# Performance work log

Measured on AMD Instinct MI355X. Metric: run time of the kernel, lower is better.

## Reference

```python
import jax, jax.numpy as jnp
import numpy as np

B, N, C = 4, 48 * 64, 256
H, W = 48, 64


def _positional_encodings(batch, dtype=jnp.float32):
    # (x^2, y^2, xy, x, y, 1) encoding; matches get_positional_encodings with intrinsics=None
    ys = jnp.linspace(-1.0, 1.0, H, dtype=dtype)
    xs = jnp.linspace(-1.0, 1.0, W, dtype=dtype)
    p3 = jnp.tile(ys, W)            # [N] : ys repeated W times (torch .repeat(B, w))
    p4 = jnp.repeat(xs, H)          # [N] : each x repeated H times (repeat_interleave)
    pos = jnp.stack([p3 * p3, p4 * p4, p3 * p4, p3, p4, jnp.ones_like(p3)], axis=-1)  # [N,6]
    return jnp.broadcast_to(pos, (batch, N, 6))


def setup_inputs() -> dict:
    key = jax.random.key(0)
    k1, k2, k3, k4 = jax.random.split(key, 4)
    x1 = jax.random.normal(k1, (B, N, C), dtype=jnp.float32)
    x2 = jax.random.normal(k2, (B, N, C), dtype=jnp.float32)
    corr = jax.random.normal(k3, (B, 1, H, W, H, W), dtype=jnp.float32)
    W_proj = jax.random.normal(k4, (C + 6, C), dtype=jnp.float32) * (1.0 / np.sqrt(C + 6))
    b_proj = jnp.zeros((C,), dtype=jnp.float32)
    return {"x1": x1, "x2": x2, "corr": corr, "W_proj": W_proj, "b_proj": b_proj}


def reference(x1, x2, corr, W_proj, b_proj):
    b, n, c = x1.shape
    a = corr.reshape(b, n, n)                      # squeeze(1) + double flatten
    # dual softmax (row-wise * column-wise)
    s_row = jax.nn.softmax(a, axis=-1)
    s_col = jax.nn.softmax(a, axis=-2)
    attn_f1 = s_row * s_col                        # [B,N,N]
    attn_f2 = jnp.swapaxes(attn_f1, -2, -1)        # softmax(a^T,-1)*softmax(a^T,-2) == attn_f1^T

    pos = _positional_encodings(b, dtype=x1.dtype)
    v1 = jnp.concatenate([x1, pos], axis=2)        # [B,N,C+6]
    v2 = jnp.concatenate([x2, pos], axis=2)

    # bilinear products v^T @ attn @ v  -> [B, C+6, C+6]
    fund1 = jnp.einsum('bnc,bnm,bmd->bcd', v1, attn_f1, v1)
    fund2 = jnp.einsum('bnc,bnm,bmd->bcd', v2, attn_f2, v2)

    fund1 = jnp.swapaxes(fund1, -2, -1)
    fund2 = jnp.swapaxes(fund2, -2, -1)

    out1 = fund1 @ W_proj + b_proj                 # proj_fundamental
    out2 = fund2 @ W_proj + b_proj
    return (out2, out1)                            # (fundamental_2, fundamental_1)
```

## Files before the change

kernel.cpp:

```cpp
#include <hip/hip_runtime.h>
#include <math.h>

#define NB 4
#define NN 3072
#define NC 256
#define CP 262
#define KG 384
#define XW 528
#define MD 272
#define K3S 8
#define HH 48
#define WW 64
#define LOG2E 1.4426950408889634f

typedef short short8 __attribute__((ext_vector_type(8)));
typedef short short4v __attribute__((ext_vector_type(4)));
typedef float f32x4 __attribute__((ext_vector_type(4)));
typedef unsigned int uint4v __attribute__((ext_vector_type(4)));

__device__ __forceinline__ float fexp2(float x) {
#if __has_builtin(__builtin_amdgcn_exp2f)
    return __builtin_amdgcn_exp2f(x);
#else
    return __exp2f(x);
#endif
}

__device__ __forceinline__ void bsplit(float v, short& h, short& l) {
    unsigned u = __float_as_uint(v);
    h = (short)(u >> 16);
    float r = v - __uint_as_float(u & 0xFFFF0000u);
    l = (short)(__float_as_uint(r) >> 16);
}

__device__ __forceinline__ void fma4(float4& c, float a, float4 b) {
    c.x = fmaf(a, b.x, c.x);
    c.y = fmaf(a, b.y, c.y);
    c.z = fmaf(a, b.z, c.z);
    c.w = fmaf(a, b.w, c.w);
}

__global__ __launch_bounds__(256) void k_stats(const float* __restrict__ corr,
                                               const float* __restrict__ x1,
                                               const float* __restrict__ x2,
                                               float* __restrict__ pM, float* __restrict__ pS,
                                               float* __restrict__ rmS, float* __restrict__ irs,
                                               short* __restrict__ Xh, short* __restrict__ Xl) {
    int bid = blockIdx.x;
    int t = threadIdx.x;
    if (bid < 384) {
        int cx = bid % 12;
        int b = (bid / 12) & 3;
        int ch = bid / 48;
        int m = cx * 256 + t;
        const float* p = corr + (size_t)b * NN * NN + (size_t)ch * 384 * NN + m;
        float mx[4], s[4];
#pragma unroll
        for (int i = 0; i < 4; i++) { mx[i] = -3.4e38f; s[i] = 0.f; }
        for (int r = 0; r < 384; r += 4) {
#pragma unroll
            for (int i = 0; i < 4; i++) {
                float x = p[(size_t)(r + i) * NN];
                float mn = fmaxf(mx[i], x);
                s[i] = s[i] * __expf(mx[i] - mn) + __expf(x - mn);
                mx[i] = mn;
            }
        }
        float mn01 = fmaxf(mx[0], mx[1]);
        float s01 = s[0] * __expf(mx[0] - mn01) + s[1] * __expf(mx[1] - mn01);
        float mn23 = fmaxf(mx[2], mx[3]);
        float s23 = s[2] * __expf(mx[2] - mn23) + s[3] * __expf(mx[3] - mn23);
        float mnA = fmaxf(mn01, mn23);
        float sA = s01 * __expf(mn01 - mnA) + s23 * __expf(mn23 - mnA);
        pM[((size_t)ch * NB + b) * NN + m] = mnA;
        pS[((size_t)ch * NB + b) * NN + m] = sA;
    } else if (bid < 3456) {
        int rid = bid - 384;
        int b = rid / 768;
        int r0 = (rid - b * 768) * 4;
        int w = t >> 6, l = t & 63;
        int n = r0 + w;
        const float4* p = (const float4*)(corr + ((size_t)b * NN + n) * NN);
        float4 v[12];
        float m = -3.4e38f;
#pragma unroll
        for (int i = 0; i < 12; i++) {
            v[i] = p[l + i * 64];
            m = fmaxf(m, fmaxf(fmaxf(v[i].x, v[i].y), fmaxf(v[i].z, v[i].w)));
        }
#pragma unroll
        for (int off = 1; off < 64; off <<= 1) m = fmaxf(m, __shfl_xor(m, off));
        float s = 0.f;
#pragma unroll
        for (int i = 0; i < 12; i++)
            s += __expf(v[i].x - m) + __expf(v[i].y - m) + __expf(v[i].z - m) + __expf(v[i].w - m);
#pragma unroll
        for (int off = 1; off < 64; off <<= 1) s += __shfl_xor(s, off);
        if (l == 0) {
            rmS[b * NN + n] = m * LOG2E;
            irs[b * NN + n] = 1.f / s;
        }
    } else {
        int id = (bid - 3456) * 256 + t;
        int col = id % XW;
        int rest = id / XW;
        int kg = rest % KG;
        int b = rest / KG;
        short* ph = Xh + (size_t)id * 8;
        short* pl = Xl + (size_t)id * 8;
        if (col < 512) {
            const float* src = (col < 256 ? x1 : x2) + ((size_t)b * NN + kg * 8) * NC + (col & 255);
#pragma unroll
            for (int j = 0; j < 8; j++) {
                short hs, ls;
                bsplit(src[(size_t)j * NC], hs, ls);
                ph[j] = hs; pl[j] = ls;
            }
        } else {
            int c = col - 512;
#pragma unroll
            for (int j = 0; j < 8; j++) {
                int k = kg * 8 + j;
                int ip4 = k / HH;
                int ip3 = k - ip4 * HH;
                float p3 = -1.f + 2.f * (float)ip3 / 47.f;
                float p4 = -1.f + 2.f * (float)ip4 / 63.f;
                float v = 0.f;
                if (c == 0) v = p3 * p3;
                else if (c == 1) v = p4 * p4;
                else if (c == 2) v = p3 * p4;
                else if (c == 3) v = p3;
                else if (c == 4) v = p4;
                else if (c == 5) v = 1.f;
                short hs, ls;
                bsplit(v, hs, ls);
                ph[j] = hs; pl[j] = ls;
            }
        }
    }
}

struct SMemMain {
    unsigned AH[2][96 * 32];
    unsigned AL[2][96 * 32];
    float ccsh[NN];
};
union SMemU {
    SMemMain m;
    float pdump[8 * 64 * 24];
};

#define LOAD_B2(PH, PL, BHF, BLF)                                           \
    {                                                                        \
        BHF[0] = *(const short8*)(PH);                                       \
        BHF[1] = *(const short8*)((PH) + 128);                               \
        BLF[0] = *(const short8*)(PL);                                       \
        BLF[1] = *(const short8*)((PL) + 128);                               \
    }

#define READ_AFRAGS6(BUFH, BUFL, UNIT, AHF, ALF)                             \
    {                                                                        \
        _Pragma("unroll") for (int fr_ = 0; fr_ < 6; fr_++) {                \
            int rowr_ = fr_ * 16 + row16;                                    \
            int uidx_ = rowr_ * 32 + (((UNIT) ^ (rowr_ & 7)) << 2);          \
            AHF[fr_] = *(const short8*)&(BUFH)[uidx_];                       \
            ALF[fr_] = *(const short8*)&(BUFL)[uidx_];                       \
        }                                                                    \
    }

#define MFMA_CLUSTER62(AHF, ALF, BHF, BLF)                                                         \
    {                                                                                              \
        _Pragma("unroll") for (int fr_ = 0; fr_ < 6; fr_++)                                        \
        _Pragma("unroll") for (int i_ = 0; i_ < 2; i_++)                                           \
            acc[fr_][i_] = __builtin_amdgcn_mfma_f32_16x16x32_bf16(AHF[fr_], BHF[i_], acc[fr_][i_], 0, 0, 0); \
        _Pragma("unroll") for (int fr_ = 0; fr_ < 6; fr_++)                                        \
        _Pragma("unroll") for (int i_ = 0; i_ < 2; i_++)                                           \
            acc[fr_][i_] = __builtin_amdgcn_mfma_f32_16x16x32_bf16(AHF[fr_], BLF[i_], acc[fr_][i_], 0, 0, 0); \
        _Pragma("unroll") for (int fr_ = 0; fr_ < 6; fr_++)                                        \
        _Pragma("unroll") for (int i_ = 0; i_ < 2; i_++)                                           \
            acc[fr_][i_] = __builtin_amdgcn_mfma_f32_16x16x32_bf16(ALF[fr_], BHF[i_], acc[fr_][i_], 0, 0, 0); \
    }

#define POS_CLUSTER6(AHF, ALF, PBH, PBL)                                                           \
    {                                                                                              \
        _Pragma("unroll") for (int fr_ = 0; fr_ < 6; fr_++) {                                      \
            accP[fr_] = __builtin_amdgcn_mfma_f32_16x16x32_bf16(AHF[fr_], (PBH), accP[fr_], 0, 0, 0); \
            accP[fr_] = __builtin_amdgcn_mfma_f32_16x16x32_bf16(AHF[fr_], (PBL), accP[fr_], 0, 0, 0); \
            accP[fr_] = __builtin_amdgcn_mfma_f32_16x16x32_bf16(ALF[fr_], (PBH), accP[fr_], 0, 0, 0); \
        }                                                                                          \
    }

#define STAGE_A(DSTH, DSTL, PC)                                                                   \
    {                                                                                             \
        f32x4 ccv0 = *(const f32x4*)&ccsh[(PC) * 64 + g * 16];                                    \
        f32x4 ccv1 = *(const f32x4*)&ccsh[(PC) * 64 + g * 16 + 4];                                \
        f32x4 ccv2 = *(const f32x4*)&ccsh[(PC) * 64 + g * 16 + 8];                                \
        f32x4 ccv3 = *(const f32x4*)&ccsh[(PC) * 64 + g * 16 + 12];                               \
        float ev[16];                                                                             \
        _Pragma("unroll") for (int q_ = 0; q_ < 4; q_++) {                                        \
            ev[q_]      = fexp2(fmaf(C2, cr[0][q_], rmn) - ccv0[q_]);                             \
            ev[4 + q_]  = fexp2(fmaf(C2, cr[1][q_], rmn) - ccv1[q_]);                             \
            ev[8 + q_]  = fexp2(fmaf(C2, cr[2][q_], rmn) - ccv2[q_]);                             \
            ev[12 + q_] = fexp2(fmaf(C2, cr[3][q_], rmn) - ccv3[q_]);                             \
        }                                                                                         \
        uint4v hi0, hi1, lo0, lo1;                                                                \
        _Pragma("unroll") for (int q_ = 0; q_ < 4; q_++) {                                        \
            unsigned u0 = __float_as_uint(ev[2 * q_]);                                            \
            unsigned u1 = __float_as_uint(ev[2 * q_ + 1]);                                        \
            hi0[q_] = __builtin_amdgcn_perm(u1, u0, 0x07060302u);                                 \
            float r0_ = ev[2 * q_] - __uint_as_float(u0 & 0xffff0000u);                           \
            float r1_ = ev[2 * q_ + 1] - __uint_as_float(u1 & 0xffff0000u);                       \
            lo0[q_] = __builtin_amdgcn_perm(__float_as_uint(r1_), __float_as_uint(r0_), 0x07060302u); \
            unsigned v0 = __float_as_uint(ev[8 + 2 * q_]);                                        \
            unsigned v1 = __float_as_uint(ev[8 + 2 * q_ + 1]);                                    \
            hi1[q_] = __builtin_amdgcn_perm(v1, v0, 0x07060302u);                                 \
            float t0_ = ev[8 + 2 * q_] - __uint_as_float(v0 & 0xffff0000u);                       \
            float t1_ = ev[8 + 2 * q_ + 1] - __uint_as_float(v1 & 0xffff0000u);                   \
            lo1[q_] = __builtin_amdgcn_perm(__float_as_uint(t1_), __float_as_uint(t0_), 0x07060302u); \
        }                                                                                         \
        *(uint4v*)&(DSTH)[widx0] = hi0;                                                           \
        *(uint4v*)&(DSTH)[widx1] = hi1;                                                           \
        *(uint4v*)&(DSTL)[widx0] = lo0;                                                           \
        *(uint4v*)&(DSTL)[widx1] = lo1;                                                           \
    }

__global__ __launch_bounds__(512, 2) void k2_mfma(const float* __restrict__ corr,
        const short* __restrict__ Xh, const short* __restrict__ Xl,
        const float* __restrict__ rmS, const float* __restrict__ irs,
        const float* __restrict__ pM, const float* __restrict__ pS,
        short* __restrict__ Zh, short* __restrict__ Zl) {
    __shared__ SMemU sm;
    float* ccsh = sm.m.ccsh;

    const float C2 = 2.f * LOG2E;
    const size_t BSTEP = (size_t)4 * XW * 8;

    int bid = blockIdx.x;
    int xcd = bid & 7, sub = bid >> 3;
    int b = xcd >> 1;
    int which = sub & 1;
    int rowblk = (xcd & 1) + ((sub >> 1) << 1);
    int n0 = rowblk * 96;

    int t = threadIdx.x;
    int w = t >> 6, l = t & 63;
    int row16 = l & 15, slot = l >> 4;
    bool doPos = (which == 0);
    bool writer = (t < 384);
    int wrow = t >> 2, g = t & 3;
    int widx0 = wrow * 32 + (((2 * g) ^ (wrow & 7)) << 2);
    int widx1 = wrow * 32 + (((2 * g + 1) ^ (wrow & 7)) << 2);

    for (int c = t; c < NN; c += 512) {
        float mx = -3.4e38f, s = 0.f;
#pragma unroll
        for (int ch = 0; ch < 8; ch++) {
            float m2 = pM[(size_t)ch * NB * NN + b * NN + c];
            float s2 = pS[(size_t)ch * NB * NN + b * NN + c];
            float mn = fmaxf(mx, m2);
            s = s * __expf(mx - mn) + s2 * __expf(m2 - mn);
            mx = mn;
        }
        ccsh[c] = fmaf(mx, LOG2E, __log2f(s));
    }

    const float* corrR = corr;
    float rmn = 0.f;
    if (writer) {
        corrR = corr + ((size_t)b * NN + n0 + wrow) * NN + g * 16;
        rmn = -rmS[b * NN + n0 + wrow];
    }

    int col0 = which * 256 + w * 32 + row16;
    const short* bh = Xh + ((size_t)(b * KG + slot) * XW + col0) * 8;
    const short* bl = Xl + ((size_t)(b * KG + slot) * XW + col0) * 8;

    f32x4 acc[6][2];
    f32x4 accP[6];
    const f32x4 zz = {0.f, 0.f, 0.f, 0.f};
#pragma unroll
    for (int fr = 0; fr < 6; fr++) {
        acc[fr][0] = zz; acc[fr][1] = zz; accP[fr] = zz;
    }

    short8 BhA[2], BlA[2], BhB[2], BlB[2];
    short8 P0h = {0,0,0,0,0,0,0,0}, P0l = P0h, P1h = P0h, P1l = P0h;
    LOAD_B2(bh, bl, BhA, BlA);

    f32x4 cr[4];
    __syncthreads();
    if (writer) {
#pragma unroll
        for (int q = 0; q < 4; q++) cr[q] = *(const f32x4*)(corrR + q * 4);
        STAGE_A(sm.m.AH[0], sm.m.AL[0], 0);
#pragma unroll
        for (int q = 0; q < 4; q++) cr[q] = *(const f32x4*)(corrR + 64 + q * 4);
    }
    asm volatile("s_waitcnt lgkmcnt(0)" ::: "memory");
    __builtin_amdgcn_s_barrier();

    int cur = 0;
    for (int p = 0; p < 48; ++p) {
        const unsigned* AHc = &sm.m.AH[cur][0];
        const unsigned* ALc = &sm.m.AL[cur][0];
        unsigned* AHn = &sm.m.AH[cur ^ 1][0];
        unsigned* ALn = &sm.m.AL[cur ^ 1][0];
        bool duty = doPos && (w == (p & 7));
        if (duty) {
            size_t o0 = ((size_t)(b * KG + p * 8 + slot) * XW + 512 + row16) * 8;
            P0h = *(const short8*)(Xh + o0);
            P0l = *(const short8*)(Xl + o0);
            P1h = *(const short8*)(Xh + o0 + BSTEP);
            P1l = *(const short8*)(Xl + o0 + BSTEP);
        }
        short8 Ah[6], Al[6];
        READ_AFRAGS6(AHc, ALc, slot, Ah, Al);
        bh += BSTEP; bl += BSTEP;
        LOAD_B2(bh, bl, BhB, BlB);
        MFMA_CLUSTER62(Ah, Al, BhA, BlA);
        if (duty) POS_CLUSTER6(Ah, Al, P0h, P0l);
        READ_AFRAGS6(AHc, ALc, 4 + slot, Ah, Al);
        if (p < 47) {
            bh += BSTEP; bl += BSTEP;
            LOAD_B2(bh, bl, BhA, BlA);
        }
        if (writer) {
            int pc = (p + 1 < 48) ? p + 1 : 47;
            STAGE_A(AHn, ALn, pc);
            int pn = (p + 2 < 48) ? p + 2 : 47;
#pragma unroll
            for (int q = 0; q < 4; q++) cr[q] = *(const f32x4*)(corrR + pn * 64 + q * 4);
        }
        MFMA_CLUSTER62(Ah, Al, BhB, BlB);
        if (duty) POS_CLUSTER6(Ah, Al, P1h, P1l);
        asm volatile("s_waitcnt lgkmcnt(0)" ::: "memory");
        __builtin_amdgcn_s_barrier();
        cur ^= 1;
    }

#pragma unroll
    for (int fr = 0; fr < 6; fr++) {
        f32x4 sv = *(const f32x4*)(irs + b * NN + n0 + fr * 16 + slot * 4);
        int kgz = rowblk * 12 + fr * 2 + (slot >> 1);
        int jb = (slot & 1) << 2;
#pragma unroll
        for (int i = 0; i < 2; i++) {
            int colv = which * 256 + w * 32 + i * 16 + row16;
            size_t off = ((size_t)(b * KG + kgz) * XW + colv) * 8 + jb;
            short4v zh, zl;
#pragma unroll
            for (int r = 0; r < 4; r++) {
                float vv = acc[fr][i][r] * sv[r];
                short hs, ls; bsplit(vv, hs, ls);
                zh[r] = hs; zl[r] = ls;
            }
            *(short4v*)(Zh + off) = zh;
            *(short4v*)(Zl + off) = zl;
        }
    }
    if (doPos) {
#pragma unroll
        for (int fr = 0; fr < 6; fr++)
            *(f32x4*)&sm.pdump[(size_t)(w * 64 + l) * 24 + fr * 4] = accP[fr];
    }
    __syncthreads();
    if (doPos && t < 384) {
        int fr = t >> 6, ll = t & 63;
        int sl = ll >> 4, r16 = ll & 15;
        f32x4 s = zz;
#pragma unroll
        for (int ww = 0; ww < 8; ww++)
            s += *(const f32x4*)&sm.pdump[(size_t)(ww * 64 + ll) * 24 + fr * 4];
        f32x4 sv = *(const f32x4*)(irs + b * NN + n0 + fr * 16 + sl * 4);
        int kgz = rowblk * 12 + fr * 2 + (sl >> 1);
        int jb = (sl & 1) << 2;
        size_t off = ((size_t)(b * KG + kgz) * XW + 512 + r16) * 8 + jb;
        short4v zh, zl;
#pragma unroll
        for (int r = 0; r < 4; r++) {
            float vv = s[r] * sv[r];
            short hs, ls; bsplit(vv, hs, ls);
            zh[r] = hs; zl[r] = ls;
        }
        *(short4v*)(Zh + off) = zh;
        *(short4v*)(Zl + off) = zl;
    }
}

__global__ __launch_bounds__(256) void k3_mfma(const short* __restrict__ Xh, const short* __restrict__ Xl,
                                               const short* __restrict__ Zh, const short* __restrict__ Zl,
                                               float* __restrict__ Mpart) {
    int tile = blockIdx.x;
    int rt = tile / 3, ct = tile % 3;
    int mb = blockIdx.y;
    int mat = mb >> 2, b = mb & 3;
    int split = blockIdx.z;

    const int O0[4] = {0, 6, 12, 17};
    int r0f = O0[rt], rNf = O0[rt + 1] - r0f;
    int c0f = O0[ct], cNf = O0[ct + 1] - c0f;

    int t = threadIdx.x;
    int w = t >> 6, l = t & 63;
    int row16 = l & 15, slot = l >> 4;
    int wr = w >> 1, wc = w & 1;
    int rh = (rNf + 1) >> 1;
    int rbeg = r0f + (wr ? rh : 0);
    int rcnt = wr ? (rNf - rh) : rh;
    int chh = (cNf + 1) >> 1;
    int cbeg = c0f + (wc ? chh : 0);
    int ccnt = wc ? (cNf - chh) : chh;

    const short *Ah_, *Al_, *Bh_, *Bl_;
    int abase, bbase;
    if (mat == 0) { Ah_ = Xh; Al_ = Xl; Bh_ = Zh; Bl_ = Zl; abase = 0; bbase = 0; }
    else          { Ah_ = Zh; Al_ = Zl; Bh_ = Xh; Bl_ = Xl; abase = 256; bbase = 256; }

    int acol[3], bcol[3];
#pragma unroll
    for (int i = 0; i < 3; i++) {
        int fa = rbeg + i;
        acol[i] = ((fa < 16) ? (abase + fa * 16) : 512) + row16;
        int fb = cbeg + i;
        bcol[i] = ((fb < 16) ? (bbase + fb * 16) : 512) + row16;
    }

    f32x4 acc[3][3];
    const f32x4 zz = {0.f, 0.f, 0.f, 0.f};
#pragma unroll
    for (int i = 0; i < 3; i++)
#pragma unroll
        for (int j = 0; j < 3; j++) acc[i][j] = zz;

    for (int it = 0; it < 12; it++) {
        int kg = split * 48 + it * 4 + slot;
        size_t base = (size_t)(b * KG + kg) * XW;
        short8 Ah[3], Al[3], Bhf[3], Blf[3];
#pragma unroll
        for (int i = 0; i < 3; i++) {
            if (i < rcnt) {
                Ah[i] = *(const short8*)(Ah_ + (base + acol[i]) * 8);
                Al[i] = *(const short8*)(Al_ + (base + acol[i]) * 8);
            }
            if (i < ccnt) {
                Bhf[i] = *(const short8*)(Bh_ + (base + bcol[i]) * 8);
                Blf[i] = *(const short8*)(Bl_ + (base + bcol[i]) * 8);
            }
        }
#pragma unroll
        for (int i = 0; i < 3; i++) {
            if (i < rcnt) {
#pragma unroll
                for (int j = 0; j < 3; j++) {
                    if (j < ccnt) {
                        acc[i][j] = __builtin_amdgcn_mfma_f32_16x16x32_bf16(Ah[i], Bhf[j], acc[i][j], 0, 0, 0);
                        acc[i][j] = __builtin_amdgcn_mfma_f32_16x16x32_bf16(Al[i], Bhf[j], acc[i][j], 0, 0, 0);
                        acc[i][j] = __builtin_amdgcn_mfma_f32_16x16x32_bf16(Ah[i], Blf[j], acc[i][j], 0, 0, 0);
                    }
                }
            }
        }
    }

    float* Mp = Mpart + (size_t)(mb * K3S + split) * (MD * MD);
#pragma unroll
    for (int i = 0; i < 3; i++) {
        if (i < rcnt) {
#pragma unroll
            for (int j = 0; j < 3; j++) {
                if (j < ccnt) {
                    int r = (rbeg + i) * 16 + slot * 4;
                    int c = (cbeg + j) * 16 + row16;
#pragma unroll
                    for (int q = 0; q < 4; q++)
                        Mp[(size_t)(r + q) * MD + c] = acc[i][j][q];
                }
            }
        }
    }
}

__global__ __launch_bounds__(256) void k_mcombine(const float* __restrict__ Mpart, float* __restrict__ M) {
    const int per = MD * MD;
    int f4 = blockIdx.x * 256 + threadIdx.x;
    if (f4 >= (8 * per) / 4) return;
    int e = f4 * 4;
    int mb = e / per;
    int off = e - mb * per;
    const float* src = Mpart + (size_t)mb * K3S * per + off;
    float4 s = make_float4(0.f, 0.f, 0.f, 0.f);
#pragma unroll
    for (int sp = 0; sp < K3S; sp++) {
        float4 v = *(const float4*)(src + (size_t)sp * per);
        s.x += v.x; s.y += v.y; s.z += v.z; s.w += v.w;
    }
    *(float4*)(M + (size_t)mb * per + off) = s;
}

__global__ __launch_bounds__(256) void k4_proj(const float* __restrict__ M, const float* __restrict__ Wp,
                                               const float* __restrict__ bp, float* __restrict__ out) {
    int i0 = blockIdx.x * 16;
    int b = blockIdx.y;
    int mat = blockIdx.z;
    const float* Mp = M + (size_t)(mat * 4 + b) * (MD * MD);
    int t = threadIdx.x;
    int jt = t & 63, it = t >> 6;
    int j = jt * 4;
    float4 a0 = make_float4(0.f, 0.f, 0.f, 0.f), a1 = a0, a2 = a0, a3 = a0;
#pragma unroll 2
    for (int k = 0; k < CP; k++) {
        float4 w = *(const float4*)(Wp + (size_t)k * NC + j);
        float4 g = *(const float4*)(Mp + (size_t)k * MD + i0 + it * 4);
        fma4(a0, g.x, w); fma4(a1, g.y, w); fma4(a2, g.z, w); fma4(a3, g.w, w);
    }
    float4 bb = *(const float4*)(bp + j);
    a0.x += bb.x; a0.y += bb.y; a0.z += bb.z; a0.w += bb.w;
    a1.x += bb.x; a1.y += bb.y; a1.z += bb.z; a1.w += bb.w;
    a2.x += bb.x; a2.y += bb.y; a2.z += bb.z; a2.w += bb.w;
    a3.x += bb.x; a3.y += bb.y; a3.z += bb.z; a3.w += bb.w;
    float* ob = out + (mat == 0 ? (size_t)NB * CP * NC : (size_t)0) + (size_t)b * CP * NC;
    int i = i0 + it * 4;
    if (i + 0 < CP) *(float4*)(ob + (size_t)(i + 0) * NC + j) = a0;
    if (i + 1 < CP) *(float4*)(ob + (size_t)(i + 1) * NC + j) = a1;
    if (i + 2 < CP) *(float4*)(ob + (size_t)(i + 2) * NC + j) = a2;
    if (i + 3 < CP) *(float4*)(ob + (size_t)(i + 3) * NC + j) = a3;
}

extern "C" void kernel_launch(void* const* d_in, const int* in_sizes, int n_in,
                              void* d_out, int out_size, void* d_ws, size_t ws_size,
                              hipStream_t stream) {
    const float* x1 = (const float*)d_in[0];
    const float* x2 = (const float*)d_in[1];
    const float* corr = (const float*)d_in[2];
    const float* Wp = (const float*)d_in[3];
    const float* bp = (const float*)d_in[4];
    float* out = (float*)d_out;
    float* w = (float*)d_ws;

    const size_t XSZ = (size_t)NB * KG * XW * 8;

    size_t o = 0;
    float* rmS = w + o;   o += NB * NN;
    float* irs = w + o;   o += NB * NN;
    float* pM = w + o;    o += 8 * NB * NN;
    float* pS = w + o;    o += 8 * NB * NN;
    short* Xh = (short*)(w + o); o += XSZ / 2;
    short* Xl = (short*)(w + o); o += XSZ / 2;
    short* Zh = (short*)(w + o); o += XSZ / 2;
    short* Zl = (short*)(w + o); o += XSZ / 2;
    float* Mpart = w + o; o += (size_t)8 * K3S * MD * MD;
    float* M = w + o;     o += (size_t)8 * MD * MD;

    k_stats<<<dim3(6624), dim3(256), 0, stream>>>(corr, x1, x2, pM, pS, rmS, irs, Xh, Xl);
    k2_mfma<<<dim3(256), dim3(512), 0, stream>>>(corr, Xh, Xl, rmS, irs, pM, pS, Zh, Zl);
    k3_mfma<<<dim3(9, 8, K3S), dim3(256), 0, stream>>>(Xh, Xl, Zh, Zl, Mpart);
    k_mcombine<<<dim3(578), dim3(256), 0, stream>>>(Mpart, M);
    k4_proj<<<dim3(17, NB, 2), dim3(256), 0, stream>>>(M, Wp, bp, out);
}
```

Measured before the change: 256.4 us.

## Fuse row and column softmax stats into one corr pass, halve k2 row tiles

The stats kernel now computes column and row partial max/sum over the same 192x256 tile of corr, so corr is read once instead of twice for statistics. A new combine kernel merges the partials into the column log-sum-exp, row max and inverse row sum. k2 is retiled from 96 to 48 rows per block with double the grid and higher occupancy, and its positional MFMA work moves to two fixed warps. k3 split-K is halved to K3S=4, which means fewer partial sums to combine but longer loops per block. The cost is an extra launch and more partial-stat traffic.

New measurement: 345.2 us. 1.35x slower.

```diff
diff --git a/kernel.cpp b/kernel.cpp
--- a/kernel.cpp
+++ b/kernel.cpp
@@ -8,7 +8,7 @@
 #define KG 384
 #define XW 528
 #define MD 272
-#define K3S 8
+#define K3S 4
 #define HH 48
 #define WW 64
 #define LOG2E 1.4426950408889634f
@@ -44,20 +44,20 @@
                                                const float* __restrict__ x1,
                                                const float* __restrict__ x2,
                                                float* __restrict__ pM, float* __restrict__ pS,
-                                               float* __restrict__ rmS, float* __restrict__ irs,
+                                               float* __restrict__ rpM, float* __restrict__ rpS,
                                                short* __restrict__ Xh, short* __restrict__ Xl) {
     int bid = blockIdx.x;
     int t = threadIdx.x;
-    if (bid < 384) {
+    if (bid < 768) {
         int cx = bid % 12;
         int b = (bid / 12) & 3;
         int ch = bid / 48;
         int m = cx * 256 + t;
-        const float* p = corr + (size_t)b * NN * NN + (size_t)ch * 384 * NN + m;
+        const float* p = corr + (size_t)b * NN * NN + (size_t)ch * 192 * NN + m;
         float mx[4], s[4];
 #pragma unroll
         for (int i = 0; i < 4; i++) { mx[i] = -3.4e38f; s[i] = 0.f; }
-        for (int r = 0; r < 384; r += 4) {
+        for (int r = 0; r < 192; r += 4) {
 #pragma unroll
             for (int i = 0; i < 4; i++) {
                 float x = p[(size_t)(r + i) * NN];
@@ -74,34 +74,23 @@
         float sA = s01 * __expf(mn01 - mnA) + s23 * __expf(mn23 - mnA);
         pM[((size_t)ch * NB + b) * NN + m] = mnA;
         pS[((size_t)ch * NB + b) * NN + m] = sA;
-    } else if (bid < 3456) {
-        int rid = bid - 384;
-        int b = rid / 768;
-        int r0 = (rid - b * 768) * 4;
         int w = t >> 6, l = t & 63;
-        int n = r0 + w;
-        const float4* p = (const float4*)(corr + ((size_t)b * NN + n) * NN);
-        float4 v[12];
-        float m = -3.4e38f;
-#pragma unroll
-        for (int i = 0; i < 12; i++) {
-            v[i] = p[l + i * 64];
-            m = fmaxf(m, fmaxf(fmaxf(v[i].x, v[i].y), fmaxf(v[i].z, v[i].w)));
-        }
-#pragma unroll
-        for (int off = 1; off < 64; off <<= 1) m = fmaxf(m, __shfl_xor(m, off));
-        float s = 0.f;
-#pragma unroll
-        for (int i = 0; i < 12; i++)
-            s += __expf(v[i].x - m) + __expf(v[i].y - m) + __expf(v[i].z - m) + __expf(v[i].w - m);
-#pragma unroll
-        for (int off = 1; off < 64; off <<= 1) s += __shfl_xor(s, off);
-        if (l == 0) {
-            rmS[b * NN + n] = m * LOG2E;
-            irs[b * NN + n] = 1.f / s;
+        for (int i = 0; i < 48; i++) {
+            int r = w * 48 + i;
+            float4 v = *(const float4*)(corr + ((size_t)b * NN + ch * 192 + r) * NN + cx * 256 + l * 4);
+            float m4 = fmaxf(fmaxf(v.x, v.y), fmaxf(v.z, v.w));
+#pragma unroll
+            for (int off = 1; off < 64; off <<= 1) m4 = fmaxf(m4, __shfl_xor(m4, off));
+            float se = __expf(v.x - m4) + __expf(v.y - m4) + __expf(v.z - m4) + __expf(v.w - m4);
+#pragma unroll
+            for (int off = 1; off < 64; off <<= 1) se += __shfl_xor(se, off);
+            if (l == 0) {
+                rpM[((size_t)cx * NB + b) * NN + ch * 192 + r] = m4;
+                rpS[((size_t)cx * NB + b) * NN + ch * 192 + r] = se;
+            }
         }
     } else {
-        int id = (bid - 3456) * 256 + t;
+        int id = (bid - 768) * 256 + t;
         int col = id % XW;
         int rest = id / XW;
         int kg = rest % KG;
@@ -140,14 +129,48 @@
     }
 }
 
+__global__ __launch_bounds__(256) void k_comb(const float* __restrict__ pM, const float* __restrict__ pS,
+                                              const float* __restrict__ rpM, const float* __restrict__ rpS,
+                                              float* __restrict__ ccS, float* __restrict__ rmS,
+                                              float* __restrict__ irs) {
+    int bid = blockIdx.x;
+    int t = threadIdx.x;
+    if (bid < 48) {
+        int idx = bid * 256 + t;
+        float mx = -3.4e38f, s = 0.f;
+#pragma unroll
+        for (int ch = 0; ch < 16; ch++) {
+            float m2 = pM[(size_t)ch * NB * NN + idx];
+            float s2 = pS[(size_t)ch * NB * NN + idx];
+            float mn = fmaxf(mx, m2);
+            s = s * __expf(mx - mn) + s2 * __expf(m2 - mn);
+            mx = mn;
+        }
+        ccS[idx] = fmaf(mx, LOG2E, __log2f(s));
+    } else {
+        int idx = (bid - 48) * 256 + t;
+        float mx = -3.4e38f, s = 0.f;
+#pragma unroll
+        for (int ch = 0; ch < 12; ch++) {
+            float m2 = rpM[(size_t)ch * NB * NN + idx];
+            float s2 = rpS[(size_t)ch * NB * NN + idx];
+            float mn = fmaxf(mx, m2);
+            s = s * __expf(mx - mn) + s2 * __expf(m2 - mn);
+            mx = mn;
+        }
+        rmS[idx] = mx * LOG2E;
+        irs[idx] = 1.f / s;
+    }
+}
+
 struct SMemMain {
-    unsigned AH[2][96 * 32];
-    unsigned AL[2][96 * 32];
+    unsigned AH[2][48 * 32];
+    unsigned AL[2][48 * 32];
     float ccsh[NN];
 };
 union SMemU {
     SMemMain m;
-    float pdump[8 * 64 * 24];
+    float pdump[2 * 64 * 12];
 };
 
 #define LOAD_B2(PH, PL, BHF, BLF)                                           \
@@ -158,9 +181,9 @@
         BLF[1] = *(const short8*)((PL) + 128);                               \
     }
 
-#define READ_AFRAGS6(BUFH, BUFL, UNIT, AHF, ALF)                             \
+#define READ_AFRAGS3(BUFH, BUFL, UNIT, AHF, ALF)                             \
     {                                                                        \
-        _Pragma("unroll") for (int fr_ = 0; fr_ < 6; fr_++) {                \
+        _Pragma("unroll") for (int fr_ = 0; fr_ < 3; fr_++) {                \
             int rowr_ = fr_ * 16 + row16;                                    \
             int uidx_ = rowr_ * 32 + (((UNIT) ^ (rowr_ & 7)) << 2);          \
             AHF[fr_] = *(const short8*)&(BUFH)[uidx_];                       \
@@ -168,66 +191,54 @@
         }                                                                    \
     }
 
-#define MFMA_CLUSTER62(AHF, ALF, BHF, BLF)                                                         \
+#define MFMA_CLUSTER32(AHF, ALF, BHF, BLF)                                                         \
     {                                                                                              \
-        _Pragma("unroll") for (int fr_ = 0; fr_ < 6; fr_++)                                        \
+        _Pragma("unroll") for (int fr_ = 0; fr_ < 3; fr_++)                                        \
         _Pragma("unroll") for (int i_ = 0; i_ < 2; i_++)                                           \
             acc[fr_][i_] = __builtin_amdgcn_mfma_f32_16x16x32_bf16(AHF[fr_], BHF[i_], acc[fr_][i_], 0, 0, 0); \
-        _Pragma("unroll") for (int fr_ = 0; fr_ < 6; fr_++)                                        \
+        _Pragma("unroll") for (int fr_ = 0; fr_ < 3; fr_++)                                        \
         _Pragma("unroll") for (int i_ = 0; i_ < 2; i_++)                                           \
             acc[fr_][i_] = __builtin_amdgcn_mfma_f32_16x16x32_bf16(AHF[fr_], BLF[i_], acc[fr_][i_], 0, 0, 0); \
-        _Pragma("unroll") for (int fr_ = 0; fr_ < 6; fr_++)                                        \
+        _Pragma("unroll") for (int fr_ = 0; fr_ < 3; fr_++)                                        \
         _Pragma("unroll") for (int i_ = 0; i_ < 2; i_++)                                           \
             acc[fr_][i_] = __builtin_amdgcn_mfma_f32_16x16x32_bf16(ALF[fr_], BHF[i_], acc[fr_][i_], 0, 0, 0); \
     }
 
-#define POS_CLUSTER6(AHF, ALF, PBH, PBL)                                                           \
+#define POS_CLUSTER3(AHF, ALF, PBH, PBL)                                                           \
     {                                                                                              \
-        _Pragma("unroll") for (int fr_ = 0; fr_ < 6; fr_++) {                                      \
+        _Pragma("unroll") for (int fr_ = 0; fr_ < 3; fr_++) {                                      \
             accP[fr_] = __builtin_amdgcn_mfma_f32_16x16x32_bf16(AHF[fr_], (PBH), accP[fr_], 0, 0, 0); \
             accP[fr_] = __builtin_amdgcn_mfma_f32_16x16x32_bf16(AHF[fr_], (PBL), accP[fr_], 0, 0, 0); \
             accP[fr_] = __builtin_amdgcn_mfma_f32_16x16x32_bf16(ALF[fr_], (PBH), accP[fr_], 0, 0, 0); \
         }                                                                                          \
     }
 
-#define STAGE_A(DSTH, DSTL, PC)                                                                   \
+#define STAGE_A8(DSTH, DSTL, PC)                                                                  \
     {                                                                                             \
-        f32x4 ccv0 = *(const f32x4*)&ccsh[(PC) * 64 + g * 16];                                    \
-        f32x4 ccv1 = *(const f32x4*)&ccsh[(PC) * 64 + g * 16 + 4];                                \
-        f32x4 ccv2 = *(const f32x4*)&ccsh[(PC) * 64 + g * 16 + 8];                                \
-        f32x4 ccv3 = *(const f32x4*)&ccsh[(PC) * 64 + g * 16 + 12];                               \
-        float ev[16];                                                                             \
+        f32x4 ccv0 = *(const f32x4*)&ccsh[(PC) * 64 + g * 8];                                     \
+        f32x4 ccv1 = *(const f32x4*)&ccsh[(PC) * 64 + g * 8 + 4];                                 \
+        float ev[8];                                                                              \
         _Pragma("unroll") for (int q_ = 0; q_ < 4; q_++) {                                        \
-            ev[q_]      = fexp2(fmaf(C2, cr[0][q_], rmn) - ccv0[q_]);                             \
-            ev[4 + q_]  = fexp2(fmaf(C2, cr[1][q_], rmn) - ccv1[q_]);                             \
-            ev[8 + q_]  = fexp2(fmaf(C2, cr[2][q_], rmn) - ccv2[q_]);                             \
-            ev[12 + q_] = fexp2(fmaf(C2, cr[3][q_], rmn) - ccv3[q_]);                             \
+            ev[q_]     = fexp2(fmaf(C2, cr0[q_], rmn) - ccv0[q_]);                                \
+            ev[4 + q_] = fexp2(fmaf(C2, cr1[q_], rmn) - ccv1[q_]);                                \
         }                                                                                         \
-        uint4v hi0, hi1, lo0, lo1;                                                                \
+        uint4v hi, lo;                                                                            \
         _Pragma("unroll") for (int q_ = 0; q_ < 4; q_++) {                                        \
             unsigned u0 = __float_as_uint(ev[2 * q_]);                                            \
             unsigned u1 = __float_as_uint(ev[2 * q_ + 1]);                                        \
-            hi0[q_] = __builtin_amdgcn_perm(u1, u0, 0x07060302u);                                 \
+            hi[q_] = __builtin_amdgcn_perm(u1, u0, 0x07060302u);                                  \
             float r0_ = ev[2 * q_] - __uint_as_float(u0 & 0xffff0000u);                           \
             float r1_ = ev[2 * q_ + 1] - __uint_as_float(u1 & 0xffff0000u);                       \
-            lo0[q_] = __builtin_amdgcn_perm(__float_as_uint(r1_), __float_as_uint(r0_), 0x07060302u); \
-            unsigned v0 = __float_as_uint(ev[8 + 2 * q_]);                                        \
-            unsigned v1 = __float_as_uint(ev[8 + 2 * q_ + 1]);                                    \
-            hi1[q_] = __builtin_amdgcn_perm(v1, v0, 0x07060302u);                                 \
-            float t0_ = ev[8 + 2 * q_] - __uint_as_float(v0 & 0xffff0000u);                       \
-            float t1_ = ev[8 + 2 * q_ + 1] - __uint_as_float(v1 & 0xffff0000u);                   \
-            lo1[q_] = __builtin_amdgcn_perm(__float_as_uint(t1_), __float_as_uint(t0_), 0x07060302u); \
+            lo[q_] = __builtin_amdgcn_perm(__float_as_uint(r1_), __float_as_uint(r0_), 0x07060302u); \
         }                                                                                         \
-        *(uint4v*)&(DSTH)[widx0] = hi0;                                                           \
-        *(uint4v*)&(DSTH)[widx1] = hi1;                                                           \
-        *(uint4v*)&(DSTL)[widx0] = lo0;                                                           \
-        *(uint4v*)&(DSTL)[widx1] = lo1;                                                           \
-    }
-
-__global__ __launch_bounds__(512, 2) void k2_mfma(const float* __restrict__ corr,
+        *(uint4v*)&(DSTH)[widx] = hi;                                                             \
+        *(uint4v*)&(DSTL)[widx] = lo;                                                             \
+    }
+
+__global__ __launch_bounds__(512, 4) void k2_mfma(const float* __restrict__ corr,
         const short* __restrict__ Xh, const short* __restrict__ Xl,
         const float* __restrict__ rmS, const float* __restrict__ irs,
-        const float* __restrict__ pM, const float* __restrict__ pS,
+        const float* __restrict__ ccS,
         short* __restrict__ Zh, short* __restrict__ Zl) {
     __shared__ SMemU sm;
     float* ccsh = sm.m.ccsh;
@@ -240,34 +251,27 @@
     int b = xcd >> 1;
     int which = sub & 1;
     int rowblk = (xcd & 1) + ((sub >> 1) << 1);
-    int n0 = rowblk * 96;
+    int n0 = rowblk * 48;
 
     int t = threadIdx.x;
     int w = t >> 6, l = t & 63;
     int row16 = l & 15, slot = l >> 4;
     bool doPos = (which == 0);
+    bool duty6 = doPos && (w == 6);
+    bool duty7 = doPos && (w == 7);
     bool writer = (t < 384);
-    int wrow = t >> 2, g = t & 3;
-    int widx0 = wrow * 32 + (((2 * g) ^ (wrow & 7)) << 2);
-    int widx1 = wrow * 32 + (((2 * g + 1) ^ (wrow & 7)) << 2);
-
-    for (int c = t; c < NN; c += 512) {
-        float mx = -3.4e38f, s = 0.f;
-#pragma unroll
-        for (int ch = 0; ch < 8; ch++) {
-            float m2 = pM[(size_t)ch * NB * NN + b * NN + c];
-            float s2 = pS[(size_t)ch * NB * NN + b * NN + c];
-            float mn = fmaxf(mx, m2);
-            s = s * __expf(mx - mn) + s2 * __expf(m2 - mn);
-            mx = mn;
-        }
-        ccsh[c] = fmaf(mx, LOG2E, __log2f(s));
+    int wrow = t >> 3, g = t & 7;
+    int widx = wrow * 32 + ((g ^ (wrow & 7)) << 2);
+
+    {
+        const f32x4* src = (const f32x4*)(ccS + (size_t)b * NN);
+        for (int i = t; i < NN / 4; i += 512) ((f32x4*)ccsh)[i] = src[i];
     }
 
     const float* corrR = corr;
     float rmn = 0.f;
     if (writer) {
-        corrR = corr + ((size_t)b * NN + n0 + wrow) * NN + g * 16;
+        corrR = corr + ((size_t)b * NN + n0 + wrow) * NN + g * 8;
         rmn = -rmS[b * NN + n0 + wrow];
     }
 
@@ -275,11 +279,11 @@
     const short* bh = Xh + ((size_t)(b * KG + slot) * XW + col0) * 8;
     const short* bl = Xl + ((size_t)(b * KG + slot) * XW + col0) * 8;
 
-    f32x4 acc[6][2];
-    f32x4 accP[6];
+    f32x4 acc[3][2];
+    f32x4 accP[3];
     const f32x4 zz = {0.f, 0.f, 0.f, 0.f};
 #pragma unroll
-    for (int fr = 0; fr < 6; fr++) {
+    for (int fr = 0; fr < 3; fr++) {
         acc[fr][0] = zz; acc[fr][1] = zz; accP[fr] = zz;
     }
 
@@ -287,14 +291,14 @@
     short8 P0h = {0,0,0,0,0,0,0,0}, P0l = P0h, P1h = P0h, P1l = P0h;
     LOAD_B2(bh, bl, BhA, BlA);
 
-    f32x4 cr[4];
+    f32x4 cr0, cr1;
     __syncthreads();
     if (writer) {
-#pragma unroll
-        for (int q = 0; q < 4; q++) cr[q] = *(const f32x4*)(corrR + q * 4);
-        STAGE_A(sm.m.AH[0], sm.m.AL[0], 0);
-#pragma unroll
-        for (int q = 0; q < 4; q++) cr[q] = *(const f32x4*)(corrR + 64 + q * 4);
+        cr0 = *(const f32x4*)(corrR);
+        cr1 = *(const f32x4*)(corrR + 4);
+        STAGE_A8(sm.m.AH[0], sm.m.AL[0], 0);
+        cr0 = *(const f32x4*)(corrR + 64);
+        cr1 = *(const f32x4*)(corrR + 68);
     }
     asm volatile("s_waitcnt lgkmcnt(0)" ::: "memory");
     __builtin_amdgcn_s_barrier();
@@ -305,43 +309,45 @@
         const unsigned* ALc = &sm.m.AL[cur][0];
         unsigned* AHn = &sm.m.AH[cur ^ 1][0];
         unsigned* ALn = &sm.m.AL[cur ^ 1][0];
-        bool duty = doPos && (w == (p & 7));
-        if (duty) {
+        short8 Ah[3], Al[3];
+        READ_AFRAGS3(AHc, ALc, slot, Ah, Al);
+        bh += BSTEP; bl += BSTEP;
+        LOAD_B2(bh, bl, BhB, BlB);
+        if (duty6) {
             size_t o0 = ((size_t)(b * KG + p * 8 + slot) * XW + 512 + row16) * 8;
             P0h = *(const short8*)(Xh + o0);
             P0l = *(const short8*)(Xl + o0);
-            P1h = *(const short8*)(Xh + o0 + BSTEP);
-            P1l = *(const short8*)(Xl + o0 + BSTEP);
-        }
-        short8 Ah[6], Al[6];
-        READ_AFRAGS6(AHc, ALc, slot, Ah, Al);
-        bh += BSTEP; bl += BSTEP;
-        LOAD_B2(bh, bl, BhB, BlB);
-        MFMA_CLUSTER62(Ah, Al, BhA, BlA);
-        if (duty) POS_CLUSTER6(Ah, Al, P0h, P0l);
-        READ_AFRAGS6(AHc, ALc, 4 + slot, Ah, Al);
+        }
+        MFMA_CLUSTER32(Ah, Al, BhA, BlA);
+        if (duty6) POS_CLUSTER3(Ah, Al, P0h, P0l);
+        READ_AFRAGS3(AHc, ALc, 4 + slot, Ah, Al);
         if (p < 47) {
             bh += BSTEP; bl += BSTEP;
             LOAD_B2(bh, bl, BhA, BlA);
         }
+        if (duty7) {
+            size_t o1 = ((size_t)(b * KG + p * 8 + 4 + slot) * XW + 512 + row16) * 8;
+            P1h = *(const short8*)(Xh + o1);
+            P1l = *(const short8*)(Xl + o1);
+        }
         if (writer) {
             int pc = (p + 1 < 48) ? p + 1 : 47;
-            STAGE_A(AHn, ALn, pc);
+            STAGE_A8(AHn, ALn, pc);
             int pn = (p + 2 < 48) ? p + 2 : 47;
-#pragma unroll
-            for (int q = 0; q < 4; q++) cr[q] = *(const f32x4*)(corrR + pn * 64 + q * 4);
-        }
-        MFMA_CLUSTER62(Ah, Al, BhB, BlB);
-        if (duty) POS_CLUSTER6(Ah, Al, P1h, P1l);
+            cr0 = *(const f32x4*)(corrR + pn * 64);
+            cr1 = *(const f32x4*)(corrR + pn * 64 + 4);
+        }
+        MFMA_CLUSTER32(Ah, Al, BhB, BlB);
+        if (duty7) POS_CLUSTER3(Ah, Al, P1h, P1l);
         asm volatile("s_waitcnt lgkmcnt(0)" ::: "memory");
         __builtin_amdgcn_s_barrier();
         cur ^= 1;
     }
 
 #pragma unroll
-    for (int fr = 0; fr < 6; fr++) {
+    for (int fr = 0; fr < 3; fr++) {
         f32x4 sv = *(const f32x4*)(irs + b * NN + n0 + fr * 16 + slot * 4);
-        int kgz = rowblk * 12 + fr * 2 + (slot >> 1);
+        int kgz = rowblk * 6 + fr * 2 + (slot >> 1);
         int jb = (slot & 1) << 2;
 #pragma unroll
         for (int i = 0; i < 2; i++) {
@@ -358,21 +364,19 @@
             *(short4v*)(Zl + off) = zl;
         }
     }
-    if (doPos) {
-#pragma unroll
-        for (int fr = 0; fr < 6; fr++)
-            *(f32x4*)&sm.pdump[(size_t)(w * 64 + l) * 24 + fr * 4] = accP[fr];
+    if (doPos && w >= 6) {
+#pragma unroll
+        for (int fr = 0; fr < 3; fr++)
+            *(f32x4*)&sm.pdump[(size_t)((w - 6) * 64 + l) * 12 + fr * 4] = accP[fr];
     }
     __syncthreads();
-    if (doPos && t < 384) {
+    if (doPos && t < 192) {
         int fr = t >> 6, ll = t & 63;
         int sl = ll >> 4, r16 = ll & 15;
-        f32x4 s = zz;
-#pragma unroll
-        for (int ww = 0; ww < 8; ww++)
-            s += *(const f32x4*)&sm.pdump[(size_t)(ww * 64 + ll) * 24 + fr * 4];
+        f32x4 s = *(const f32x4*)&sm.pdump[(size_t)ll * 12 + fr * 4]
+                + *(const f32x4*)&sm.pdump[(size_t)(64 + ll) * 12 + fr * 4];
         f32x4 sv = *(const f32x4*)(irs + b * NN + n0 + fr * 16 + sl * 4);
-        int kgz = rowblk * 12 + fr * 2 + (sl >> 1);
+        int kgz = rowblk * 6 + fr * 2 + (sl >> 1);
         int jb = (sl & 1) << 2;
         size_t off = ((size_t)(b * KG + kgz) * XW + 512 + r16) * 8 + jb;
         short4v zh, zl;
@@ -432,8 +436,8 @@
 #pragma unroll
         for (int j = 0; j < 3; j++) acc[i][j] = zz;
 
-    for (int it = 0; it < 12; it++) {
-        int kg = split * 48 + it * 4 + slot;
+    for (int it = 0; it < 24; it++) {
+        int kg = split * 96 + it * 4 + slot;
         size_t base = (size_t)(b * KG + kg) * XW;
         short8 Ah[3], Al[3], Bhf[3], Blf[3];
 #pragma unroll
@@ -542,8 +546,11 @@
     size_t o = 0;
     float* rmS = w + o;   o += NB * NN;
     float* irs = w + o;   o += NB * NN;
-    float* pM = w + o;    o += 8 * NB * NN;
-    float* pS = w + o;    o += 8 * NB * NN;
+    float* ccS = w + o;   o += NB * NN;
+    float* pM = w + o;    o += 16 * NB * NN;
+    float* pS = w + o;    o += 16 * NB * NN;
+    float* rpM = w + o;   o += 12 * NB * NN;
+    float* rpS = w + o;   o += 12 * NB * NN;
     short* Xh = (short*)(w + o); o += XSZ / 2;
     short* Xl = (short*)(w + o); o += XSZ / 2;
     short* Zh = (short*)(w + o); o += XSZ / 2;
@@ -551,8 +558,9 @@
     float* Mpart = w + o; o += (size_t)8 * K3S * MD * MD;
     float* M = w + o;     o += (size_t)8 * MD * MD;
 
-    k_stats<<<dim3(6624), dim3(256), 0, stream>>>(corr, x1, x2, pM, pS, rmS, irs, Xh, Xl);
-    k2_mfma<<<dim3(256), dim3(512), 0, stream>>>(corr, Xh, Xl, rmS, irs, pM, pS, Zh, Zl);
+    k_stats<<<dim3(3936), dim3(256), 0, stream>>>(corr, x1, x2, pM, pS, rpM, rpS, Xh, Xl);
+    k_comb<<<dim3(96), dim3(256), 0, stream>>>(pM, pS, rpM, rpS, ccS, rmS, irs);
+    k2_mfma<<<dim3(512), dim3(512), 0, stream>>>(corr, Xh, Xl, rmS, irs, ccS, Zh, Zl);
     k3_mfma<<<dim3(9, 8, K3S), dim3(256), 0, stream>>>(Xh, Xl, Zh, Zl, Mpart);
     k_mcombine<<<dim3(578), dim3(256), 0, stream>>>(Mpart, M);
     k4_proj<<<dim3(17, NB, 2), dim3(256), 0, stream>>>(M, Wp, bp, out);
```
